# Optimization experiments

Measured on AMD Instinct MI355X. Metric: run time of the kernel, lower is better.

## Reference

```python
import jax, jax.numpy as jnp
import numpy as np
from jax import lax

B_SZ, L, D_MODEL = 2, 2048, 1024
D_INNER, D_STATE, D_CONV, DT_RANK = 2048, 16, 4, 64


def setup_inputs() -> dict:
    key = jax.random.key(0)
    ks = jax.random.split(key, 9)
    s = 0.02
    x = jax.random.normal(ks[0], (B_SZ, L, D_MODEL), dtype=jnp.float32)
    W_in = jax.random.normal(ks[1], (D_MODEL, 2 * D_INNER), dtype=jnp.float32) * s
    conv_w = jax.random.normal(ks[2], (D_INNER, D_CONV), dtype=jnp.float32) * s
    conv_b = jax.random.normal(ks[3], (D_INNER,), dtype=jnp.float32) * s
    W_x = jax.random.normal(ks[4], (D_INNER, DT_RANK + 2 * D_STATE), dtype=jnp.float32) * s
    W_dt = jax.random.normal(ks[5], (DT_RANK, D_INNER), dtype=jnp.float32) * s
    b_dt = jax.random.normal(ks[6], (D_INNER,), dtype=jnp.float32) * s
    A_log = jnp.log(jnp.broadcast_to(jnp.arange(1, D_STATE + 1, dtype=jnp.float32), (D_INNER, D_STATE)))
    D = jnp.ones((D_INNER,), dtype=jnp.float32)
    W_out = jax.random.normal(ks[7], (D_INNER, D_MODEL), dtype=jnp.float32) * s
    return {"x": x, "W_in": W_in, "conv_w": conv_w, "conv_b": conv_b,
            "W_x": W_x, "W_dt": W_dt, "b_dt": b_dt, "A_log": A_log, "D": D, "W_out": W_out}


def _silu(v):
    return v * jax.nn.sigmoid(v)


def _mamba_fwd(x, W_in, conv_w, conv_b, W_x, W_dt, b_dt, A_log, D, W_out):
    b, l, _ = x.shape
    xz = x @ W_in                                  # [b,l,2*d_inner]
    xs, res = jnp.split(xz, 2, axis=-1)
    # causal depthwise conv1d (torch pads d_conv-1 both sides then truncates to l -> left pad only)
    xc = xs.transpose(0, 2, 1)                     # [b,d_inner,l]
    xc = lax.conv_general_dilated(
        xc, conv_w[:, None, :], window_strides=(1,),
        padding=[(D_CONV - 1, 0)], feature_group_count=D_INNER,
        dimension_numbers=("NCH", "OIH", "NCH")) + conv_b[None, :, None]
    u = _silu(xc.transpose(0, 2, 1))               # [b,l,d_inner]
    # projections for delta, B, C
    x_dbl = u @ W_x                                # [b,l,dt_rank+2n]
    dt, Bm, Cm = jnp.split(x_dbl, [DT_RANK, DT_RANK + D_STATE], axis=-1)
    delta = jax.nn.softplus(dt @ W_dt + b_dt)      # [b,l,d_inner]
    A = -jnp.exp(A_log)                            # [d_inner,n]

    def step(h, inp):
        d_t, B_t, C_t, u_t = inp                   # [b,d_in],[b,n],[b,n],[b,d_in]
        dA = jnp.exp(d_t[:, :, None] * A)          # [b,d_in,n]
        h = dA * h + d_t[:, :, None] * B_t[:, None, :] * u_t[:, :, None]
        y = jnp.einsum("bdn,bn->bd", h, C_t)
        return h, y

    h0 = jnp.zeros((b, D_INNER, D_STATE), dtype=u.dtype)
    _, ys = lax.scan(step, h0, (delta.transpose(1, 0, 2), Bm.transpose(1, 0, 2),
                                Cm.transpose(1, 0, 2), u.transpose(1, 0, 2)))
    y = ys.transpose(1, 0, 2) + u * D              # [b,l,d_inner]
    y = y * _silu(res)
    return y @ W_out                               # [b,l,d_model]


def reference(x, W_in, conv_w, conv_b, W_x, W_dt, b_dt, A_log, D, W_out):
    return _mamba_fwd(x, W_in, conv_w, conv_b, W_x, W_dt, b_dt, A_log, D, W_out)
```

## Files before the change

### kernel.cpp

```cpp
#include <hip/hip_runtime.h>
#include <hip/hip_bf16.h>
#include <math.h>

#define B_SZ    2
#define LSEQ    2048
#define DMODEL  1024
#define DINNER  2048
#define DSTATE  16
#define DCONV   4
#define DTRANK  64

#define NCHUNK  64
#define CLEN    (LSEQ / NCHUNK)

#define KSPLIT  16
#define NX      96

typedef unsigned short u16;
typedef __bf16 bf16x8 __attribute__((ext_vector_type(8)));
typedef float  f32x4  __attribute__((ext_vector_type(4)));

static __device__ __forceinline__ float sigmoidf_(float x) {
    return 1.0f / (1.0f + __expf(-x));
}
static __device__ __forceinline__ u16 f2b(float f) {
    unsigned int u = __float_as_uint(f);
    u = (u + 0x7fffu + ((u >> 16) & 1u)) >> 16;
    return (u16)u;
}
static __device__ __forceinline__ float b2f(u16 v) {
    return __uint_as_float(((unsigned int)v) << 16);
}

__global__ __launch_bounds__(256) void cast_bf16(
    const float* __restrict__ in, u16* __restrict__ out, int n8)
{
    const int i = blockIdx.x * 256 + threadIdx.x;
    if (i >= n8) return;
    const float4* p = reinterpret_cast<const float4*>(in + (size_t)i * 8);
    float4 v0 = p[0], v1 = p[1];
    union { u16 u[8]; uint4 q; } r;
    r.u[0] = f2b(v0.x); r.u[1] = f2b(v0.y); r.u[2] = f2b(v0.z); r.u[3] = f2b(v0.w);
    r.u[4] = f2b(v1.x); r.u[5] = f2b(v1.y); r.u[6] = f2b(v1.z); r.u[7] = f2b(v1.w);
    reinterpret_cast<uint4*>(out)[i] = r.q;
}

__global__ __launch_bounds__(256) void castT_bf16(
    const float* __restrict__ in, u16* __restrict__ out, int R, int C)
{
    __shared__ float t[32][33];
    const int r0 = blockIdx.y * 32, c0 = blockIdx.x * 32;
    const int tr = threadIdx.x >> 3;
    const int tc4 = (threadIdx.x & 7) * 4;
    const float4 v = *reinterpret_cast<const float4*>(in + (size_t)(r0 + tr) * C + c0 + tc4);
    t[tr][tc4 + 0] = v.x; t[tr][tc4 + 1] = v.y; t[tr][tc4 + 2] = v.z; t[tr][tc4 + 3] = v.w;
    __syncthreads();
    union { u16 u[4]; uint2 q; } r;
    #pragma unroll
    for (int j = 0; j < 4; j++) r.u[j] = f2b(t[tc4 + j][tr]);
    *reinterpret_cast<uint2*>(out + (size_t)(c0 + tr) * R + r0 + tc4) = r.q;
}

template<int EPI>
__global__ __launch_bounds__(256) void gemm_mfma(
    const u16* __restrict__ A, const u16* __restrict__ Bt,
    float* __restrict__ Cf, u16* __restrict__ o0, u16* __restrict__ o1,
    const float* __restrict__ bias, int M, int N, int K, int ldc)
{
    __shared__ u16 As[128 * 32];
    __shared__ u16 Bs[128 * 32];
    const int tid  = threadIdx.x;
    const int lane = tid & 63;
    const int wave = tid >> 6;
    const int wr = wave >> 1, wc = wave & 1;
    const int bm = blockIdx.y * 128, bn = blockIdx.x * 128;
    const int lhi = lane >> 4;
    const int llo = lane & 15;

    f32x4 acc[4][4] = {};

    const int rs = (lhi ^ ((llo >> 1) & 3)) * 8;

    for (int k0 = 0; k0 < K; k0 += 32) {
        #pragma unroll
        for (int c = 0; c < 2; ++c) {
            const int s   = c * 256 + wave * 64 + lane;
            const int row = s >> 2, seg = s & 3;
            const int sseg = seg ^ ((row >> 1) & 3);
            const u16* ga = A  + (size_t)(bm + row) * K + k0 + sseg * 8;
            const u16* gb = Bt + (size_t)(bn + row) * K + k0 + sseg * 8;
            __builtin_amdgcn_global_load_lds(
                (const __attribute__((address_space(1))) void*)ga,
                (__attribute__((address_space(3))) void*)(As + (size_t)(c * 256 + wave * 64) * 8),
                16, 0, 0);
            __builtin_amdgcn_global_load_lds(
                (const __attribute__((address_space(1))) void*)gb,
                (__attribute__((address_space(3))) void*)(Bs + (size_t)(c * 256 + wave * 64) * 8),
                16, 0, 0);
        }
        __syncthreads();

        bf16x8 af[4], bfr[4];
        #pragma unroll
        for (int m = 0; m < 4; ++m)
            af[m] = *reinterpret_cast<const bf16x8*>(&As[(wr * 64 + m * 16 + llo) * 32 + rs]);
        #pragma unroll
        for (int n = 0; n < 4; ++n)
            bfr[n] = *reinterpret_cast<const bf16x8*>(&Bs[(wc * 64 + n * 16 + llo) * 32 + rs]);
        #pragma unroll
        for (int m = 0; m < 4; ++m)
            #pragma unroll
            for (int n = 0; n < 4; ++n)
                acc[m][n] = __builtin_amdgcn_mfma_f32_16x16x32_bf16(af[m], bfr[n], acc[m][n], 0, 0, 0);
        __syncthreads();
    }

    #pragma unroll
    for (int m = 0; m < 4; ++m) {
        const int row0 = bm + wr * 64 + m * 16 + lhi * 4;
        #pragma unroll
        for (int n = 0; n < 4; ++n) {
            const int col = bn + wc * 64 + n * 16 + llo;
            #pragma unroll
            for (int j = 0; j < 4; ++j) {
                float v = acc[m][n][j];
                if (EPI == 0) {
                    Cf[(size_t)(row0 + j) * ldc + col] = v;
                } else if (EPI == 1) {
                    if (col < DINNER) {
                        o0[(size_t)(row0 + j) * DINNER + col] = f2b(v);
                    } else {
                        v = v * sigmoidf_(v);
                        o1[(size_t)(row0 + j) * DINNER + (col - DINNER)] = f2b(v);
                    }
                } else {
                    v += bias[col];
                    v = (v > 20.f) ? v : log1pf(__expf(v));
                    o0[(size_t)(row0 + j) * ldc + col] = f2b(v);
                }
            }
        }
    }
}

__global__ __launch_bounds__(256) void conv_silu_bf(
    const u16* __restrict__ xs, const float* __restrict__ conv_w,
    const float* __restrict__ conv_b, u16* __restrict__ u)
{
    const int g  = blockIdx.x * 256 + threadIdx.x;
    const int d8 = (g & 255) * 8;
    const int bl = g >> 8;
    const int l  = bl & (LSEQ - 1);

    float4 wv[8];
    #pragma unroll
    for (int j = 0; j < 8; j++)
        wv[j] = *reinterpret_cast<const float4*>(conv_w + (size_t)(d8 + j) * DCONV);

    float acc[8];
    #pragma unroll
    for (int j = 0; j < 8; j++) acc[j] = conv_b[d8 + j];

    #pragma unroll
    for (int k = 0; k < DCONV; k++) {
        const int l2 = l - (DCONV - 1) + k;
        if (l2 < 0) continue;
        const uint4 q = *reinterpret_cast<const uint4*>(
            xs + (size_t)(bl - (DCONV - 1) + k) * DINNER + d8);
        const u16* e = reinterpret_cast<const u16*>(&q);
        #pragma unroll
        for (int j = 0; j < 8; j++) {
            const float w = (k == 0) ? wv[j].x : (k == 1) ? wv[j].y : (k == 2) ? wv[j].z : wv[j].w;
            acc[j] = fmaf(b2f(e[j]), w, acc[j]);
        }
    }
    union { u16 u[8]; uint4 q; } r;
    #pragma unroll
    for (int j = 0; j < 8; j++) {
        const float v = acc[j];
        r.u[j] = f2b(v * sigmoidf_(v));
    }
    *reinterpret_cast<uint4*>(u + (size_t)bl * DINNER + d8) = r.q;
}

__global__ __launch_bounds__(256) void gemm3_splitk(
    const u16* __restrict__ ubf, const float* __restrict__ Wx,
    float* __restrict__ partial)
{
    __shared__ float us[64][65];
    __shared__ float wsm[64][96];

    const int tid = threadIdx.x;
    const int r0 = blockIdx.x * 64;
    const int k0 = blockIdx.y * (DINNER / KSPLIT);

    const int orow = tid >> 2;
    const int oc0  = (tid & 3) * 24;

    float acc[24];
    #pragma unroll
    for (int j = 0; j < 24; j++) acc[j] = 0.f;

    for (int ks = 0; ks < DINNER / KSPLIT; ks += 64) {
        {
            const int row = tid >> 2;
            const int c16 = (tid & 3) << 4;
            const uint4* src = reinterpret_cast<const uint4*>(
                ubf + (size_t)(r0 + row) * DINNER + k0 + ks + c16);
            const uint4 q0 = src[0], q1 = src[1];
            const u16* e0 = reinterpret_cast<const u16*>(&q0);
            const u16* e1 = reinterpret_cast<const u16*>(&q1);
            #pragma unroll
            for (int j = 0; j < 8; j++) us[row][c16 + j]     = b2f(e0[j]);
            #pragma unroll
            for (int j = 0; j < 8; j++) us[row][c16 + 8 + j] = b2f(e1[j]);
        }
        #pragma unroll
        for (int j = 0; j < 6; j++) {
            const int fid = tid + j * 256;
            const int kr  = fid / 24;
            const int c4  = (fid % 24) * 4;
            *reinterpret_cast<float4*>(&wsm[kr][c4]) =
                *reinterpret_cast<const float4*>(Wx + (size_t)(k0 + ks + kr) * NX + c4);
        }
        __syncthreads();

        for (int kk = 0; kk < 64; ++kk) {
            const float uv = us[orow][kk];
            #pragma unroll
            for (int j = 0; j < 24; j++)
                acc[j] = fmaf(uv, wsm[kk][oc0 + j], acc[j]);
        }
        __syncthreads();
    }

    float* pp = partial + ((size_t)blockIdx.y * (B_SZ * LSEQ) + r0 + orow) * NX + oc0;
    #pragma unroll
    for (int j = 0; j < 24; j += 4)
        *reinterpret_cast<float4*>(pp + j) = make_float4(acc[j], acc[j+1], acc[j+2], acc[j+3]);
}

__global__ __launch_bounds__(256) void gemm3_reduce(
    const float* __restrict__ partial, float* __restrict__ xdbl,
    u16* __restrict__ x64bf)
{
    const int i = blockIdx.x * 256 + threadIdx.x;
    if (i >= B_SZ * LSEQ * NX / 4) return;
    float4 s = make_float4(0.f, 0.f, 0.f, 0.f);
    #pragma unroll
    for (int p = 0; p < KSPLIT; p++) {
        const float4 v = reinterpret_cast<const float4*>(
            partial + (size_t)p * (B_SZ * LSEQ) * NX)[i];
        s.x += v.x; s.y += v.y; s.z += v.z; s.w += v.w;
    }
    reinterpret_cast<float4*>(xdbl)[i] = s;

    const int col4 = (i % 24) * 4;
    if (col4 < DTRANK) {
        const int row = i / 24;
        union { u16 u[4]; uint2 q; } r;
        r.u[0] = f2b(s.x); r.u[1] = f2b(s.y); r.u[2] = f2b(s.z); r.u[3] = f2b(s.w);
        *reinterpret_cast<uint2*>(x64bf + (size_t)row * DTRANK + col4) = r.q;
    }
}

__global__ __launch_bounds__(256) void scan_phase1(
    const u16* __restrict__ dl_bf, const u16* __restrict__ ubf,
    const float* __restrict__ xdbl, const float* __restrict__ A_log,
    float* __restrict__ hend, float* __restrict__ Sd)
{
    const int idx = blockIdx.x * 256 + threadIdx.x;
    const int d = idx & (DINNER - 1);
    const int c = (idx >> 11) & (NCHUNK - 1);
    const int b = idx >> 17;

    float a[DSTATE];
    #pragma unroll
    for (int n = 0; n < DSTATE; n++) a[n] = -__expf(A_log[d * DSTATE + n]);

    float h[DSTATE];
    #pragma unroll
    for (int n = 0; n < DSTATE; n++) h[n] = 0.f;
    float sd = 0.f;

    const int l0 = b * LSEQ + c * CLEN;
    for (int i = 0; i < CLEN; ++i) {
        const size_t r = (size_t)(l0 + i);
        const float dv = b2f(dl_bf[r * DINNER + d]);
        const float uv = b2f(ubf[r * DINNER + d]);
        sd += dv;
        float Bv[DSTATE];
        {
            const float4* bp = reinterpret_cast<const float4*>(xdbl + r * NX + DTRANK);
            float4 q;
            q = bp[0]; Bv[0]=q.x;  Bv[1]=q.y;  Bv[2]=q.z;  Bv[3]=q.w;
            q = bp[1]; Bv[4]=q.x;  Bv[5]=q.y;  Bv[6]=q.z;  Bv[7]=q.w;
            q = bp[2]; Bv[8]=q.x;  Bv[9]=q.y;  Bv[10]=q.z; Bv[11]=q.w;
            q = bp[3]; Bv[12]=q.x; Bv[13]=q.y; Bv[14]=q.z; Bv[15]=q.w;
        }
        const float du = dv * uv;
        #pragma unroll
        for (int n = 0; n < DSTATE; n++)
            h[n] = fmaf(__expf(dv * a[n]), h[n], du * Bv[n]);
    }

    float* hp = hend + ((size_t)(b * DINNER + d) * NCHUNK + c) * DSTATE;
    #pragma unroll
    for (int n = 0; n < DSTATE; n += 4)
        *reinterpret_cast<float4*>(hp + n) = make_float4(h[n], h[n+1], h[n+2], h[n+3]);
    Sd[(size_t)(b * DINNER + d) * NCHUNK + c] = sd;
}

__global__ __launch_bounds__(256) void scan_phase2(
    float* __restrict__ hend, const float* __restrict__ Sd,
    const float* __restrict__ A_log)
{
    const int idx = blockIdx.x * 256 + threadIdx.x;
    if (idx >= B_SZ * DINNER * DSTATE) return;
    const int n = idx & (DSTATE - 1);
    const int d = (idx >> 4) & (DINNER - 1);
    const int b = idx >> 15;

    const float an = -__expf(A_log[d * DSTATE + n]);
    const size_t base = (size_t)(b * DINNER + d) * NCHUNK;
    float carry = 0.f;
    for (int c = 0; c < NCHUNK; ++c) {
        const float P = __expf(an * Sd[base + c]);
        const size_t off = (base + c) * DSTATE + n;
        const float tmp = hend[off];
        hend[off] = carry;
        carry = fmaf(P, carry, tmp);
    }
}

__global__ __launch_bounds__(256) void scan_phase3(
    const u16* __restrict__ dl_bf, const u16* __restrict__ ubf,
    const u16* __restrict__ zs_bf, const float* __restrict__ xdbl,
    const float* __restrict__ A_log, const float* __restrict__ Dp,
    const float* __restrict__ hin, u16* __restrict__ ybf)
{
    const int idx = blockIdx.x * 256 + threadIdx.x;
    const int d = idx & (DINNER - 1);
    const int c = (idx >> 11) & (NCHUNK - 1);
    const int b = idx >> 17;

    float a[DSTATE];
    #pragma unroll
    for (int n = 0; n < DSTATE; n++) a[n] = -__expf(A_log[d * DSTATE + n]);
    const float Dd = Dp[d];

    float h[DSTATE];
    {
        const float* hp = hin + ((size_t)(b * DINNER + d) * NCHUNK + c) * DSTATE;
        #pragma unroll
        for (int n = 0; n < DSTATE; n += 4) {
            const float4 t = *reinterpret_cast<const float4*>(hp + n);
            h[n] = t.x; h[n+1] = t.y; h[n+2] = t.z; h[n+3] = t.w;
        }
    }

    const int l0 = b * LSEQ + c * CLEN;
    for (int i = 0; i < CLEN; ++i) {
        const size_t r = (size_t)(l0 + i);
        const float dv = b2f(dl_bf[r * DINNER + d]);
        const float uv = b2f(ubf[r * DINNER + d]);

        const float4* bp = reinterpret_cast<const float4*>(xdbl + r * NX + DTRANK);
        float Bv[DSTATE], Cv[DSTATE];
        {
            float4 t;
            t = bp[0]; Bv[0]=t.x;  Bv[1]=t.y;  Bv[2]=t.z;  Bv[3]=t.w;
            t = bp[1]; Bv[4]=t.x;  Bv[5]=t.y;  Bv[6]=t.z;  Bv[7]=t.w;
            t = bp[2]; Bv[8]=t.x;  Bv[9]=t.y;  Bv[10]=t.z; Bv[11]=t.w;
            t = bp[3]; Bv[12]=t.x; Bv[13]=t.y; Bv[14]=t.z; Bv[15]=t.w;
            t = bp[4]; Cv[0]=t.x;  Cv[1]=t.y;  Cv[2]=t.z;  Cv[3]=t.w;
            t = bp[5]; Cv[4]=t.x;  Cv[5]=t.y;  Cv[6]=t.z;  Cv[7]=t.w;
            t = bp[6]; Cv[8]=t.x;  Cv[9]=t.y;  Cv[10]=t.z; Cv[11]=t.w;
            t = bp[7]; Cv[12]=t.x; Cv[13]=t.y; Cv[14]=t.z; Cv[15]=t.w;
        }

        const float du = dv * uv;
        float yv = 0.f;
        #pragma unroll
        for (int n = 0; n < DSTATE; n++) {
            h[n] = fmaf(__expf(dv * a[n]), h[n], du * Bv[n]);
            yv = fmaf(h[n], Cv[n], yv);
        }
        yv = fmaf(uv, Dd, yv);

        const float g = b2f(zs_bf[r * DINNER + d]);
        ybf[r * DINNER + d] = f2b(yv * g);
    }
}

extern "C" void kernel_launch(void* const* d_in, const int* in_sizes, int n_in,
                              void* d_out, int out_size, void* d_ws, size_t ws_size,
                              hipStream_t stream) {
    const float* x      = (const float*)d_in[0];
    const float* W_in   = (const float*)d_in[1];
    const float* conv_w = (const float*)d_in[2];
    const float* conv_b = (const float*)d_in[3];
    const float* W_x    = (const float*)d_in[4];
    const float* W_dt   = (const float*)d_in[5];
    const float* b_dt   = (const float*)d_in[6];
    const float* A_log  = (const float*)d_in[7];
    const float* Dp     = (const float*)d_in[8];
    const float* W_out  = (const float*)d_in[9];
    float* out = (float*)d_out;

    const int M = B_SZ * LSEQ;

    float* ws     = (float*)d_ws;
    float* xdbl   = ws;
    float* hend   = xdbl + (size_t)M * NX;
    float* Sd     = hend + (size_t)B_SZ * DINNER * NCHUNK * DSTATE;
    float* part   = Sd   + (size_t)B_SZ * DINNER * NCHUNK;
    u16*   xs_bf  = (u16*)(part + (size_t)KSPLIT * M * NX);
    u16*   zs_bf  = xs_bf + (size_t)M * DINNER;
    u16*   u_bf   = zs_bf + (size_t)M * DINNER;
    u16*   dl_bf  = u_bf  + (size_t)M * DINNER;
    u16*   xbf    = dl_bf + (size_t)M * DINNER;
    u16*   WinT   = xbf   + (size_t)M * DMODEL;
    u16*   WoutT  = WinT  + (size_t)M * DMODEL;
    u16*   x64bf  = WoutT + (size_t)DMODEL * DINNER;
    u16*   WdtT   = x64bf + (size_t)M * DTRANK;
    u16*   ybf    = xbf;

    dim3 blk(256);

    cast_bf16<<<dim3((M * DMODEL / 8) / 256), blk, 0, stream>>>(x, xbf, M * DMODEL / 8);
    castT_bf16<<<dim3((2 * DINNER) / 32, DMODEL / 32), blk, 0, stream>>>(
        W_in, WinT, DMODEL, 2 * DINNER);

    gemm_mfma<1><<<dim3((2 * DINNER) / 128, M / 128), blk, 0, stream>>>(
        xbf, WinT, nullptr, xs_bf, zs_bf, nullptr, M, 2 * DINNER, DMODEL, 0);

    conv_silu_bf<<<dim3((M * DINNER / 8) / 256), blk, 0, stream>>>(
        xs_bf, conv_w, conv_b, u_bf);

    gemm3_splitk<<<dim3(M / 64, KSPLIT), blk, 0, stream>>>(u_bf, W_x, part);
    gemm3_reduce<<<dim3((M * NX / 4 + 255) / 256), blk, 0, stream>>>(part, xdbl, x64bf);

    castT_bf16<<<dim3(DINNER / 32, DTRANK / 32), blk, 0, stream>>>(
        W_dt, WdtT, DTRANK, DINNER);
    gemm_mfma<2><<<dim3(DINNER / 128, M / 128), blk, 0, stream>>>(
        x64bf, WdtT, nullptr, dl_bf, nullptr, b_dt, M, DINNER, DTRANK, DINNER);

    scan_phase1<<<dim3((B_SZ * DINNER * NCHUNK) / 256), blk, 0, stream>>>(
        dl_bf, u_bf, xdbl, A_log, hend, Sd);
    scan_phase2<<<dim3((B_SZ * DINNER * DSTATE) / 256), blk, 0, stream>>>(
        hend, Sd, A_log);
    scan_phase3<<<dim3((B_SZ * DINNER * NCHUNK) / 256), blk, 0, stream>>>(
        dl_bf, u_bf, zs_bf, xdbl, A_log, Dp, hend, ybf);

    castT_bf16<<<dim3(DMODEL / 32, DINNER / 32), blk, 0, stream>>>(
        W_out, WoutT, DINNER, DMODEL);

    gemm_mfma<0><<<dim3(DMODEL / 128, M / 128), blk, 0, stream>>>(
        ybf, WoutT, out, nullptr, nullptr, nullptr, M, DMODEL, DINNER, DMODEL);
}
```

Baseline: 408.8 us.

## Replace input projection GEMM with 256x256 double-buffered direct-to-LDS MFMA kernel

The input projection GEMM moves from a 128x128 tile, 4-wave kernel to a 256x256 tile, 8-wave kernel. Tiles are loaded straight from global memory into LDS through global_load_lds with an XOR swizzle, and the K loop is double-buffered. The loop is split into four MFMA phases with setprio and explicit barriers so the next tile's loads overlap compute. The aim is more data reuse per tile and less load latency in the largest GEMM. In exchange it uses 128 KB of LDS per block, runs one block per CU, and launches only 16x16 blocks, which may leave some CUs idle.

```diff
diff --git a/kernel.cpp b/kernel.cpp
--- a/kernel.cpp
+++ b/kernel.cpp
@@ -59,6 +59,144 @@
     #pragma unroll
     for (int j = 0; j < 4; j++) r.u[j] = f2b(t[tc4 + j][tr]);
     *reinterpret_cast<uint2*>(out + (size_t)(c0 + tr) * R + r0 + tc4) = r.q;
+}
+
+__global__ __launch_bounds__(512, 1) void gemm1_8ph(
+    const u16* __restrict__ A, const u16* __restrict__ Bt,
+    u16* __restrict__ xs_bf, u16* __restrict__ zs_bf)
+{
+    extern __shared__ u16 smem[];
+    const int tid  = threadIdx.x;
+    const int lane = tid & 63;
+    const int wave = tid >> 6;
+    const int wr = wave >> 2, wc = wave & 3;
+    const int bm = blockIdx.y * 256, bn = blockIdx.x * 256;
+    const int lhi = lane >> 4, llo = lane & 15;
+    constexpr int K  = DMODEL;
+    constexpr int NT = K / 64;
+
+    const int lrow8 = lane >> 3;
+    const int gsrc  = ((lane & 7) ^ lrow8) * 8;
+
+    f32x4 acc[8][4] = {};
+
+    auto stage = [&](int kt, int buf) {
+        #pragma unroll
+        for (int h = 0; h < 2; ++h)
+            #pragma unroll
+            for (int i = 0; i < 2; ++i) {
+                const int rowb = h * 128 + i * 64 + wave * 8;
+                const int o16  = buf * 16384 + h * 8192 + i * 4096 + wave * 512;
+                const u16* ga = A + (size_t)(bm + rowb + lrow8) * K + kt * 64 + gsrc;
+                __builtin_amdgcn_global_load_lds(
+                    (const __attribute__((address_space(1))) void*)ga,
+                    (__attribute__((address_space(3))) void*)(smem + o16), 16, 0, 0);
+                const u16* gb = Bt + (size_t)(bn + rowb + lrow8) * K + kt * 64 + gsrc;
+                __builtin_amdgcn_global_load_lds(
+                    (const __attribute__((address_space(1))) void*)gb,
+                    (__attribute__((address_space(3))) void*)(smem + 32768 + o16), 16, 0, 0);
+            }
+    };
+    auto lda = [&](int m, int ks, int buf) -> bf16x8 {
+        const int row = wr * 128 + m * 16 + llo;
+        const int g   = (ks * 4 + lhi) ^ (llo & 7);
+        return *reinterpret_cast<const bf16x8*>(smem + buf * 16384 + row * 64 + g * 8);
+    };
+    auto ldb = [&](int n, int ks, int buf) -> bf16x8 {
+        const int row = wc * 64 + n * 16 + llo;
+        const int g   = (ks * 4 + lhi) ^ (llo & 7);
+        return *reinterpret_cast<const bf16x8*>(smem + 32768 + buf * 16384 + row * 64 + g * 8);
+    };
+
+    stage(0, 0);
+    stage(1, 1);
+    asm volatile("s_waitcnt vmcnt(8)" ::: "memory");
+    __builtin_amdgcn_s_barrier();
+
+    #pragma unroll 2
+    for (int t = 0; t < NT; ++t) {
+        const int cur = t & 1;
+        bf16x8 afr[4][2], bf0[2][2], bf1[2][2];
+
+        #pragma unroll
+        for (int m = 0; m < 4; ++m) { afr[m][0] = lda(m, 0, cur); afr[m][1] = lda(m, 1, cur); }
+        #pragma unroll
+        for (int n = 0; n < 2; ++n) { bf0[n][0] = ldb(n, 0, cur); bf0[n][1] = ldb(n, 1, cur); }
+        __builtin_amdgcn_s_setprio(1);
+        #pragma unroll
+        for (int m = 0; m < 4; ++m)
+            #pragma unroll
+            for (int n = 0; n < 2; ++n) {
+                acc[m][n] = __builtin_amdgcn_mfma_f32_16x16x32_bf16(afr[m][0], bf0[n][0], acc[m][n], 0, 0, 0);
+                acc[m][n] = __builtin_amdgcn_mfma_f32_16x16x32_bf16(afr[m][1], bf0[n][1], acc[m][n], 0, 0, 0);
+            }
+        __builtin_amdgcn_s_setprio(0);
+
+        #pragma unroll
+        for (int n = 0; n < 2; ++n) { bf1[n][0] = ldb(2 + n, 0, cur); bf1[n][1] = ldb(2 + n, 1, cur); }
+        __builtin_amdgcn_s_setprio(1);
+        #pragma unroll
+        for (int m = 0; m < 4; ++m)
+            #pragma unroll
+            for (int n = 0; n < 2; ++n) {
+                acc[m][2 + n] = __builtin_amdgcn_mfma_f32_16x16x32_bf16(afr[m][0], bf1[n][0], acc[m][2 + n], 0, 0, 0);
+                acc[m][2 + n] = __builtin_amdgcn_mfma_f32_16x16x32_bf16(afr[m][1], bf1[n][1], acc[m][2 + n], 0, 0, 0);
+            }
+        __builtin_amdgcn_s_setprio(0);
+
+        #pragma unroll
+        for (int m = 0; m < 4; ++m) { afr[m][0] = lda(4 + m, 0, cur); afr[m][1] = lda(4 + m, 1, cur); }
+        __builtin_amdgcn_s_setprio(1);
+        #pragma unroll
+        for (int m = 0; m < 4; ++m)
+            #pragma unroll
+            for (int n = 0; n < 2; ++n) {
+                acc[4 + m][2 + n] = __builtin_amdgcn_mfma_f32_16x16x32_bf16(afr[m][0], bf1[n][0], acc[4 + m][2 + n], 0, 0, 0);
+                acc[4 + m][2 + n] = __builtin_amdgcn_mfma_f32_16x16x32_bf16(afr[m][1], bf1[n][1], acc[4 + m][2 + n], 0, 0, 0);
+            }
+        __builtin_amdgcn_s_setprio(0);
+
+        __builtin_amdgcn_sched_barrier(0);
+        __builtin_amdgcn_s_barrier();
+        __builtin_amdgcn_sched_barrier(0);
+
+        if (t + 2 < NT) stage(t + 2, cur);
+        __builtin_amdgcn_s_setprio(1);
+        #pragma unroll
+        for (int m = 0; m < 4; ++m)
+            #pragma unroll
+            for (int n = 0; n < 2; ++n) {
+                acc[4 + m][n] = __builtin_amdgcn_mfma_f32_16x16x32_bf16(afr[m][0], bf0[n][0], acc[4 + m][n], 0, 0, 0);
+                acc[4 + m][n] = __builtin_amdgcn_mfma_f32_16x16x32_bf16(afr[m][1], bf0[n][1], acc[4 + m][n], 0, 0, 0);
+            }
+        __builtin_amdgcn_s_setprio(0);
+
+        __builtin_amdgcn_sched_barrier(0);
+        if (t + 2 < NT) { asm volatile("s_waitcnt vmcnt(8)" ::: "memory"); }
+        else            { asm volatile("s_waitcnt vmcnt(0)" ::: "memory"); }
+        __builtin_amdgcn_s_barrier();
+        __builtin_amdgcn_sched_barrier(0);
+    }
+
+    const bool is_xs = (bn < DINNER);
+    #pragma unroll
+    for (int m = 0; m < 8; ++m) {
+        const int row0 = bm + wr * 128 + m * 16 + lhi * 4;
+        #pragma unroll
+        for (int n = 0; n < 4; ++n) {
+            const int col = bn + wc * 64 + n * 16 + llo;
+            #pragma unroll
+            for (int j = 0; j < 4; ++j) {
+                float v = acc[m][n][j];
+                if (is_xs) {
+                    xs_bf[(size_t)(row0 + j) * DINNER + col] = f2b(v);
+                } else {
+                    v = v * sigmoidf_(v);
+                    zs_bf[(size_t)(row0 + j) * DINNER + (col - DINNER)] = f2b(v);
+                }
+            }
+        }
+    }
 }
 
 template<int EPI>
@@ -126,13 +264,6 @@
                 float v = acc[m][n][j];
                 if (EPI == 0) {
                     Cf[(size_t)(row0 + j) * ldc + col] = v;
-                } else if (EPI == 1) {
-                    if (col < DINNER) {
-                        o0[(size_t)(row0 + j) * DINNER + col] = f2b(v);
-                    } else {
-                        v = v * sigmoidf_(v);
-                        o1[(size_t)(row0 + j) * DINNER + (col - DINNER)] = f2b(v);
-                    }
                 } else {
                     v += bias[col];
                     v = (v > 20.f) ? v : log1pf(__expf(v));
@@ -432,8 +563,8 @@
     castT_bf16<<<dim3((2 * DINNER) / 32, DMODEL / 32), blk, 0, stream>>>(
         W_in, WinT, DMODEL, 2 * DINNER);
 
-    gemm_mfma<1><<<dim3((2 * DINNER) / 128, M / 128), blk, 0, stream>>>(
-        xbf, WinT, nullptr, xs_bf, zs_bf, nullptr, M, 2 * DINNER, DMODEL, 0);
+    gemm1_8ph<<<dim3((2 * DINNER) / 256, M / 256), dim3(512), 131072, stream>>>(
+        xbf, WinT, xs_bf, zs_bf);
 
     conv_silu_bf<<<dim3((M * DINNER / 8) / 256), blk, 0, stream>>>(
         xs_bf, conv_w, conv_b, u_bf);
```

Measured after the change: 389.0 us. 4.8% less time.
